# Performance work log

Hardware: AMD Instinct MI355X
Metric: run time of the kernel (lower is better)

The kernel has to match this reference:

```python
import jax, jax.numpy as jnp
import numpy as np

B, S, D, M = 4, 2048, 1024, 4  # batch, seq_len, d_model, n_stride_masks


def setup_inputs() -> dict:
    key = jax.random.key(0)
    ks = jax.random.split(key, 10)
    lin = lambda k: jax.random.normal(k, (D, D), jnp.float32) / np.float32(np.sqrt(D))
    return {
        "x": jax.random.normal(ks[0], (B, S, D), jnp.float32),
        "stride_masks": jax.random.randint(ks[1], (M, S, S), 0, 2, jnp.int32),
        "Wq": lin(ks[2]), "bq": jnp.zeros((D,), jnp.float32),
        "Wk": lin(ks[3]), "bk": jnp.zeros((D,), jnp.float32),
        "Wv": lin(ks[4]), "bv": jnp.zeros((D,), jnp.float32),
        "Wo": lin(ks[5]), "bo": jnp.zeros((D,), jnp.float32),
    }


def reference(x, stride_masks, Wq, bq, Wk, bk, Wv, bv, Wo, bo):
    scale = jnp.float32(np.sqrt(D))
    Q = x @ Wq + bq  # [B,S,D]
    K = x @ Wk + bk
    V = x @ Wv + bv
    # scores are identical for every mask; compute once (same math as the loop)
    scores = jnp.einsum("bqd,bkd->bqk", Q, K) / scale  # [B,S,S]
    masked = jnp.where(stride_masks[:, None] == 0, jnp.float32(-1e9), scores[None])  # [M,B,S,S]
    weights = jax.nn.softmax(masked, axis=-1)
    # sum over masks then divide by M == mean(stack(outs), 0)
    out = jnp.einsum("mbqk,bkd->bqd", weights, V) / jnp.float32(M)
    return out @ Wo + bo
```

## Files before the change

kernel.cpp:

```cpp
#include <hip/hip_runtime.h>
#include <hip/hip_bf16.h>
#include <stdint.h>

#define B_ 4
#define S_ 2048
#define D_ 1024
#define M_ 4

typedef __bf16 bf16;
typedef _Float16 f16;
typedef __bf16 bf16x8 __attribute__((ext_vector_type(8)));
typedef _Float16 f16x8 __attribute__((ext_vector_type(8)));
typedef float f32x4 __attribute__((ext_vector_type(4)));

__device__ __forceinline__ void async_copy16(const void* g, void* l) {
  __builtin_amdgcn_global_load_lds(
      (const __attribute__((address_space(1))) void*)g,
      (__attribute__((address_space(3))) void*)l, 16, 0, 0);
}

__global__ __launch_bounds__(256) void convert_copy(const float* __restrict__ in,
                                                    bf16* __restrict__ out, long n) {
  const long i = ((long)blockIdx.x * blockDim.x + threadIdx.x) * 8;
  if (i >= n) return;
  const float4 a = *(const float4*)(in + i);
  const float4 b = *(const float4*)(in + i + 4);
  bf16x8 o;
  o[0] = (bf16)a.x; o[1] = (bf16)a.y; o[2] = (bf16)a.z; o[3] = (bf16)a.w;
  o[4] = (bf16)b.x; o[5] = (bf16)b.y; o[6] = (bf16)b.z; o[7] = (bf16)b.w;
  *(bf16x8*)(out + i) = o;
}

__global__ __launch_bounds__(256) void transposeW4(
    const float* __restrict__ w0, const float* __restrict__ w1,
    const float* __restrict__ w2, const float* __restrict__ w3,
    bf16* __restrict__ out) {
  __shared__ bf16 t[64][65];
  const float* in = (blockIdx.z == 0) ? w0 : (blockIdx.z == 1) ? w1
                    : (blockIdx.z == 2) ? w2 : w3;
  out += (long)blockIdx.z * D_ * D_;
  const int r0 = blockIdx.y * 64;
  const int c0 = blockIdx.x * 64;
  const int tx = threadIdx.x & 63;
  const int ty = threadIdx.x >> 6;
#pragma unroll
  for (int i = ty; i < 64; i += 4)
    t[i][tx] = (bf16)in[(long)(r0 + i) * D_ + c0 + tx];
  __syncthreads();
#pragma unroll
  for (int i = ty; i < 64; i += 4) out[(long)(c0 + i) * D_ + r0 + tx] = t[tx][i];
}

__global__ __launch_bounds__(256) void pack_masks(const int* __restrict__ masks,
                                                  unsigned char* __restrict__ pk) {
  const long SS = (long)S_ * S_;
  const long e = ((long)blockIdx.x * 256 + threadIdx.x) * 8;
  unsigned long long w = 0;
#pragma unroll
  for (int m = 0; m < M_; ++m) {
    const int4 a = *(const int4*)(masks + m * SS + e);
    const int4 b = *(const int4*)(masks + m * SS + e + 4);
    const int v[8] = {a.x, a.y, a.z, a.w, b.x, b.y, b.z, b.w};
#pragma unroll
    for (int j = 0; j < 8; ++j)
      w |= (unsigned long long)(v[j] != 0 ? 1u : 0u) << (8 * j + m);
  }
  *(unsigned long long*)(pk + e) = w;
}

#define MODE_PLAIN 0
#define MODE_EXP 1
#define MODE_QKV 2

template <typename OutT, int MODE>
__global__ __launch_bounds__(256) void gemm_bt(
    const bf16* __restrict__ A, long aB, int lda,
    const bf16* __restrict__ Bt, long bB, int ldb,
    OutT* __restrict__ C, long cB, int ldc,
    const float* __restrict__ bias0, const float* __restrict__ bias1,
    const float* __restrict__ bias2, float alpha, int K) {
  __shared__ __align__(16) bf16 As[128 * 64];
  __shared__ __align__(16) bf16 Bs[128 * 64];
  const int tid = threadIdx.x;
  const int lane = tid & 63;
  const int w = tid >> 6;
  const int wm = w & 1;
  const int wn = w >> 1;
  A += (long)blockIdx.z * aB;
  Bt += (long)blockIdx.z * bB;
  if (MODE != MODE_QKV) C += (long)blockIdx.z * cB;
  const int row0 = blockIdx.y * 128;
  const int col0 = blockIdx.x * 128;
  const int quad = lane >> 4;
  const int l15 = lane & 15;
  const int srow = lane >> 3;
  const int scol = (lane & 7) * 8;

  f32x4 acc[4][4];
#pragma unroll
  for (int i = 0; i < 4; ++i)
#pragma unroll
    for (int j = 0; j < 4; ++j) acc[i][j] = (f32x4){0.f, 0.f, 0.f, 0.f};

  for (int kt = 0; kt < K; kt += 64) {
#pragma unroll
    for (int c = 0; c < 4; ++c) {
      const int r = c * 32 + w * 8;
      async_copy16(A + (long)(row0 + r + srow) * lda + kt + scol, &As[r * 64]);
      async_copy16(Bt + (long)(col0 + r + srow) * ldb + kt + scol, &Bs[r * 64]);
    }
    __syncthreads();
#pragma unroll
    for (int ks = 0; ks < 2; ++ks) {
      bf16x8 af[4], bf[4];
#pragma unroll
      for (int i = 0; i < 4; ++i) {
        af[i] = *(const bf16x8*)&As[(wm * 64 + i * 16 + l15) * 64 + ks * 32 + quad * 8];
        bf[i] = *(const bf16x8*)&Bs[(wn * 64 + i * 16 + l15) * 64 + ks * 32 + quad * 8];
      }
#pragma unroll
      for (int mi = 0; mi < 4; ++mi)
#pragma unroll
        for (int ni = 0; ni < 4; ++ni)
          acc[mi][ni] = __builtin_amdgcn_mfma_f32_16x16x32_bf16(af[mi], bf[ni], acc[mi][ni], 0, 0, 0);
    }
    __syncthreads();
  }

  const int grp = (MODE == MODE_QKV) ? (blockIdx.x >> 3) : 0;
  const float* bias = (MODE == MODE_QKV)
                          ? (grp == 0 ? bias0 : grp == 1 ? bias1 : bias2)
                          : bias0;
  const long NX = (long)B_ * S_ * D_;

#pragma unroll
  for (int mi = 0; mi < 4; ++mi)
#pragma unroll
    for (int ni = 0; ni < 4; ++ni) {
      const int col = col0 + wn * 64 + ni * 16 + l15;
      const int lcol = col & (D_ - 1);
      const float bv = bias ? bias[MODE == MODE_QKV ? lcol : col] : 0.0f;
#pragma unroll
      for (int r = 0; r < 4; ++r) {
        const int row = row0 + wm * 64 + mi * 16 + quad * 4 + r;
        const float val = acc[mi][ni][r] * alpha + bv;
        if (MODE == MODE_EXP) {
          C[(long)row * ldc + col] = (OutT)__expf(val);
        } else if (MODE == MODE_QKV) {
          if (grp < 2) {
            C[grp * NX + (long)row * D_ + lcol] = (OutT)val;
          } else {
            C[2 * NX + ((long)(row >> 11) * D_ + lcol) * (long)S_ + (row & (S_ - 1))] =
                (OutT)val;
          }
        } else {
          C[(long)row * ldc + col] = (OutT)val;
        }
      }
    }
}

__global__ __launch_bounds__(256) void softmax_combine(
    const f16* __restrict__ E, const unsigned char* __restrict__ pk,
    bf16* __restrict__ P) {
  const int q = blockIdx.x;
  const int b = blockIdx.y;
  const int tid = threadIdx.x;
  const int lane = tid & 63;
  const int wv = tid >> 6;
  __shared__ float4 red[4];

  float e[8];
  {
    const f16x8 h = *(const f16x8*)(E + ((long)b * S_ + q) * S_ + tid * 8);
#pragma unroll
    for (int j = 0; j < 8; ++j) e[j] = (float)h[j];
  }
  const unsigned long long mb =
      *(const unsigned long long*)(pk + (long)q * S_ + tid * 8);

  float4 s = {0.f, 0.f, 0.f, 0.f};
#pragma unroll
  for (int j = 0; j < 8; ++j) {
    const unsigned bits = (unsigned)(mb >> (8 * j)) & 0xF;
    const float ev = e[j];
    if (bits & 1) s.x += ev;
    if (bits & 2) s.y += ev;
    if (bits & 4) s.z += ev;
    if (bits & 8) s.w += ev;
  }
#pragma unroll
  for (int o = 32; o > 0; o >>= 1) {
    s.x += __shfl_xor(s.x, o, 64);
    s.y += __shfl_xor(s.y, o, 64);
    s.z += __shfl_xor(s.z, o, 64);
    s.w += __shfl_xor(s.w, o, 64);
  }
  if (lane == 0) red[wv] = s;
  __syncthreads();
  const float4 t0 = red[0], t1 = red[1], t2 = red[2], t3 = red[3];
  const float r0 = 0.25f / (t0.x + t1.x + t2.x + t3.x);
  const float r1 = 0.25f / (t0.y + t1.y + t2.y + t3.y);
  const float r2 = 0.25f / (t0.z + t1.z + t2.z + t3.z);
  const float r3 = 0.25f / (t0.w + t1.w + t2.w + t3.w);

  bf16x8 o;
#pragma unroll
  for (int j = 0; j < 8; ++j) {
    const unsigned bits = (unsigned)(mb >> (8 * j)) & 0xF;
    const float wgt = ((bits & 1) ? r0 : 0.f) + ((bits & 2) ? r1 : 0.f) +
                      ((bits & 4) ? r2 : 0.f) + ((bits & 8) ? r3 : 0.f);
    o[j] = (bf16)(e[j] * wgt);
  }
  *(bf16x8*)(P + ((long)b * S_ + q) * S_ + tid * 8) = o;
}

extern "C" void kernel_launch(void* const* d_in, const int* in_sizes, int n_in,
                              void* d_out, int out_size, void* d_ws, size_t ws_size,
                              hipStream_t stream) {
  const float* x = (const float*)d_in[0];
  const int* masks = (const int*)d_in[1];
  const float* bq = (const float*)d_in[3];
  const float* bk = (const float*)d_in[5];
  const float* bv = (const float*)d_in[7];
  const float* bo = (const float*)d_in[9];
  float* out = (float*)d_out;

  const long DD = (long)D_ * D_;
  const long SD = (long)S_ * D_;
  const long NX = (long)B_ * SD;
  const long SS = (long)S_ * S_;

  bf16* xc = (bf16*)d_ws;
  bf16* WqT = xc + NX;
  bf16* WoT = WqT + 3 * DD;
  bf16* Q = WoT + DD;
  bf16* K = Q + NX;
  bf16* VT = K + NX;
  bf16* P = VT + NX;
  f16* E = (f16*)(P + (long)B_ * SS);
  unsigned char* pk = (unsigned char*)(E + (long)B_ * SS);
  bf16* attn = Q;

  dim3 blk(256);

  convert_copy<<<dim3((uint32_t)(NX / 8 / 256)), blk, 0, stream>>>(x, xc, NX);
  transposeW4<<<dim3(16, 16, 4), blk, 0, stream>>>(
      (const float*)d_in[2], (const float*)d_in[4],
      (const float*)d_in[6], (const float*)d_in[8], WqT);
  pack_masks<<<dim3((uint32_t)(SS / 8 / 256)), blk, 0, stream>>>(masks, pk);

  gemm_bt<bf16, MODE_QKV><<<dim3(24, 64), blk, 0, stream>>>(
      xc, 0, D_, WqT, 0, D_, Q, 0, D_, bq, bk, bv, 1.0f, D_);

  gemm_bt<f16, MODE_EXP><<<dim3(16, 16, B_), blk, 0, stream>>>(
      Q, SD, D_, K, SD, D_, E, SS, S_, nullptr, nullptr, nullptr, 1.0f / 32.0f, D_);

  softmax_combine<<<dim3(S_, B_), blk, 0, stream>>>(E, pk, P);

  gemm_bt<bf16, MODE_PLAIN><<<dim3(8, 16, B_), blk, 0, stream>>>(
      P, SS, S_, VT, SD, S_, attn, SD, D_, nullptr, nullptr, nullptr, 1.0f, S_);

  gemm_bt<float, MODE_PLAIN><<<dim3(8, 64), blk, 0, stream>>>(
      attn, 0, D_, WoT, 0, D_, out, 0, D_, bo, nullptr, nullptr, 1.0f, D_);
}
```

Measured before the change: 420.8 us.

## Group GEMM tiles for L2 reuse and move V transpose to separate kernel

Remaps the block index in the shared GEMM kernel so that consecutive blocks walk down groups of eight row tiles, which should improve L2 reuse of the A and B tiles. The QKV GEMM now writes V in row-major layout, the same as Q and K, instead of doing a strided transposed scatter in its epilogue. A new tiled LDS transpose kernel then builds VT, which costs one extra launch, one extra read and write of V, and more workspace.

Measured after the change: 413.2 us. No clear change (-1.8%).

```diff
diff --git a/kernel.cpp b/kernel.cpp
--- a/kernel.cpp
+++ b/kernel.cpp
@@ -49,6 +49,23 @@
   __syncthreads();
 #pragma unroll
   for (int i = ty; i < 64; i += 4) out[(long)(c0 + i) * D_ + r0 + tx] = t[tx][i];
+}
+
+__global__ __launch_bounds__(256) void transposeB(
+    const bf16* __restrict__ in, bf16* __restrict__ out,
+    int rows, int cols, long ib, long ob) {
+  __shared__ bf16 t[64][65];
+  in += (long)blockIdx.z * ib;
+  out += (long)blockIdx.z * ob;
+  const int r0 = blockIdx.y * 64;
+  const int c0 = blockIdx.x * 64;
+  const int tx = threadIdx.x & 63;
+  const int ty = threadIdx.x >> 6;
+#pragma unroll
+  for (int i = ty; i < 64; i += 4) t[i][tx] = in[(long)(r0 + i) * cols + c0 + tx];
+  __syncthreads();
+#pragma unroll
+  for (int i = ty; i < 64; i += 4) out[(long)(c0 + i) * rows + r0 + tx] = t[tx][i];
 }
 
 __global__ __launch_bounds__(256) void pack_masks(const int* __restrict__ masks,
@@ -89,8 +106,15 @@
   A += (long)blockIdx.z * aB;
   Bt += (long)blockIdx.z * bB;
   if (MODE != MODE_QKV) C += (long)blockIdx.z * cB;
-  const int row0 = blockIdx.y * 128;
-  const int col0 = blockIdx.x * 128;
+
+  const int gx = gridDim.x;
+  const int pid = blockIdx.y * gx + blockIdx.x;
+  const int gsz = 8 * gx;
+  const int bym = (pid / gsz) * 8 + (pid % 8);
+  const int bxm = (pid % gsz) / 8;
+
+  const int row0 = bym * 128;
+  const int col0 = bxm * 128;
   const int quad = lane >> 4;
   const int l15 = lane & 15;
   const int srow = lane >> 3;
@@ -127,7 +151,7 @@
     __syncthreads();
   }
 
-  const int grp = (MODE == MODE_QKV) ? (blockIdx.x >> 3) : 0;
+  const int grp = (MODE == MODE_QKV) ? (bxm >> 3) : 0;
   const float* bias = (MODE == MODE_QKV)
                           ? (grp == 0 ? bias0 : grp == 1 ? bias1 : bias2)
                           : bias0;
@@ -147,12 +171,7 @@
         if (MODE == MODE_EXP) {
           C[(long)row * ldc + col] = (OutT)__expf(val);
         } else if (MODE == MODE_QKV) {
-          if (grp < 2) {
-            C[grp * NX + (long)row * D_ + lcol] = (OutT)val;
-          } else {
-            C[2 * NX + ((long)(row >> 11) * D_ + lcol) * (long)S_ + (row & (S_ - 1))] =
-                (OutT)val;
-          }
+          C[grp * NX + (long)row * D_ + lcol] = (OutT)val;
         } else {
           C[(long)row * ldc + col] = (OutT)val;
         }
@@ -236,7 +255,8 @@
   bf16* WoT = WqT + 3 * DD;
   bf16* Q = WoT + DD;
   bf16* K = Q + NX;
-  bf16* VT = K + NX;
+  bf16* V = K + NX;
+  bf16* VT = V + NX;
   bf16* P = VT + NX;
   f16* E = (f16*)(P + (long)B_ * SS);
   unsigned char* pk = (unsigned char*)(E + (long)B_ * SS);
@@ -253,6 +273,8 @@
   gemm_bt<bf16, MODE_QKV><<<dim3(24, 64), blk, 0, stream>>>(
       xc, 0, D_, WqT, 0, D_, Q, 0, D_, bq, bk, bv, 1.0f, D_);
 
+  transposeB<<<dim3(16, 32, B_), blk, 0, stream>>>(V, VT, S_, D_, SD, SD);
+
   gemm_bt<f16, MODE_EXP><<<dim3(16, 16, B_), blk, 0, stream>>>(
       Q, SD, D_, K, SD, D_, E, SS, S_, nullptr, nullptr, nullptr, 1.0f / 32.0f, D_);
 
```
